# Performance work log

Measured on AMD Instinct MI355X. Metric: run time of the kernel, lower is better.

Reference implementation:

```python
import jax, jax.numpy as jnp
import numpy as np

NEG_SLOPE = 0.2


def _gatv2_layer(x, Wl, bl, Wr, br, att, bo, src, dst, N):
    """PyG GATv2Conv: lin_l on source, lin_r on target, segment softmax over dst."""
    H, C = att.shape
    xl = (x @ Wl + bl).reshape(N, H, C)  # source transform
    xr = (x @ Wr + br).reshape(N, H, C)  # target transform
    e = jax.nn.leaky_relu(xl[src] + xr[dst], NEG_SLOPE)      # [E,H,C]
    score = jnp.einsum('ehc,hc->eh', e, att)                 # [E,H]
    smax = jax.lax.stop_gradient(
        jax.ops.segment_max(score, dst, num_segments=N))     # [N,H]
    ex = jnp.exp(score - smax[dst])
    denom = jax.ops.segment_sum(ex, dst, num_segments=N)     # [N,H]
    alpha = ex / denom[dst]                                  # [E,H]
    out = jax.ops.segment_sum(xl[src] * alpha[..., None], dst, num_segments=N)
    return out.reshape(N, H * C) + bo, alpha


def setup_inputs() -> dict:
    key = jax.random.key(0)
    ks = jax.random.split(key, 24)
    N, E, F_in, Hd, H = 50000, 800000, 16, 128, 4
    C = Hd // H

    def p(k, shape, scale=0.05):
        return jax.random.normal(k, shape, jnp.float32) * scale

    inp = {
        'x': jax.random.normal(ks[0], (N, F_in), jnp.float32),
        'edge_index': jax.random.randint(ks[1], (2, E), 0, N, jnp.int32),
        'edge_attr': jax.random.normal(ks[2], (E, 4), jnp.float32),
        'batch': jnp.zeros((N,), jnp.int32),
        'enc_W': p(ks[3], (F_in, Hd)), 'enc_b': p(ks[4], (Hd,)),
        'g1_Wl': p(ks[5], (Hd, Hd)), 'g1_bl': p(ks[6], (Hd,)),
        'g1_Wr': p(ks[7], (Hd, Hd)), 'g1_br': p(ks[8], (Hd,)),
        'g1_att': p(ks[9], (H, C)), 'g1_bo': p(ks[10], (Hd,)),
        'g2_Wl': p(ks[11], (Hd, Hd)), 'g2_bl': p(ks[12], (Hd,)),
        'g2_Wr': p(ks[13], (Hd, Hd)), 'g2_br': p(ks[14], (Hd,)),
        'g2_att': p(ks[15], (H, C)), 'g2_bo': p(ks[16], (Hd,)),
        'mlp_W1': p(ks[17], (Hd, Hd)), 'mlp_b1': p(ks[18], (Hd,)),
        'mlp_W2': p(ks[19], (Hd, 1)), 'mlp_b2': p(ks[20], (1,)),
    }
    return inp


def reference(x, edge_index, edge_attr, batch,
              enc_W, enc_b,
              g1_Wl, g1_bl, g1_Wr, g1_br, g1_att, g1_bo,
              g2_Wl, g2_bl, g2_Wr, g2_br, g2_att, g2_bo,
              mlp_W1, mlp_b1, mlp_W2, mlp_b2):
    N = x.shape[0]
    # add_self_loops=True (both GAT layers)
    loops = jnp.arange(N, dtype=edge_index.dtype)
    src = jnp.concatenate([edge_index[0], loops])
    dst = jnp.concatenate([edge_index[1], loops])

    h = x @ enc_W + enc_b                                    # node_encoder
    h1, a1 = _gatv2_layer(h, g1_Wl, g1_bl, g1_Wr, g1_br, g1_att, g1_bo, src, dst, N)
    h1 = jax.nn.relu(h1)
    h2, a2 = _gatv2_layer(h1, g2_Wl, g2_bl, g2_Wr, g2_br, g2_att, g2_bo, src, dst, N)
    logits = jax.nn.relu(h2 @ mlp_W1 + mlp_b1) @ mlp_W2 + mlp_b2  # [N,1]
    probs = jax.nn.sigmoid(logits[:, 0])                     # [N]
    return probs, (a1, a2)
```

## Files before the change

### kernel.cpp

```cpp
#include <hip/hip_runtime.h>
#include <hip/hip_bf16.h>

#define NEG_SLOPE 0.2f
#define AS 136
#define CAPD 64
#define L2E 1.44269504f
#define EPB 4096

typedef __bf16 bf16x8 __attribute__((ext_vector_type(8)));
typedef float  f32x4  __attribute__((ext_vector_type(4)));

__device__ __forceinline__ float b2f(__hip_bfloat16 v) { return __bfloat162float(v); }
__device__ __forceinline__ __hip_bfloat16 f2b(float v) { return __float2bfloat16(v); }
__device__ __forceinline__ float lo16(unsigned u) { return __uint_as_float(u << 16); }
__device__ __forceinline__ float hi16(unsigned u) { return __uint_as_float(u & 0xFFFF0000u); }

template<int CTRL>
__device__ __forceinline__ float dpp_add(float p) {
    int t = __builtin_amdgcn_update_dpp(0, __float_as_int(p), CTRL, 0xF, 0xF, true);
    return p + __int_as_float(t);
}

__device__ __forceinline__ float fexp2(float x) {
    float r;
    asm("v_exp_f32 %0, %1" : "=v"(r) : "v"(x));
    return r;
}

__device__ __forceinline__ int wild16(unsigned short w) {
    int e = (w >> 7) & 0xFF;
    return (e == 0 || e >= 0xC0) ? 1 : 0;
}

__device__ __forceinline__ void store_out(void* out, size_t idx, float v, int isF32) {
    if (isF32) ((float*)out)[idx] = v;
    else       ((__hip_bfloat16*)out)[idx] = f2b(v);
}

#define NCVT 13
struct CvtTab {
    const void* src[NCVT];
    float*      dst[NCVT];
    int         n[NCVT];
    int         total;
};
struct WtTab { const void* src[5]; __hip_bfloat16* dst[5]; };

__global__ __launch_bounds__(1024) void k_pre(const int* __restrict__ ei, int E,
        int ET, int N, int shift, int nbkt, int b1, int* __restrict__ gcnt,
        CvtTab tab, WtTab wt, const unsigned short* __restrict__ det,
        int* __restrict__ FLAG) {
    __shared__ int shp[1024];
    __shared__ __hip_bfloat16 wst[1024];
    int t = threadIdx.x, b = blockIdx.x;
    if (b < b1) {
        if (t < 512) shp[t] = 0;
        __syncthreads();
        int e0 = b * EPB, e1 = min(e0 + EPB, ET);
        for (int e = e0 + t; e < e1; e += 1024) {
            int d = (e < E) ? ei[E + e] : (e - E);
            if ((unsigned)d < (unsigned)N) atomicAdd(&shp[d >> shift], 1);
        }
        __syncthreads();
        for (int i = t; i < nbkt; i += 1024) gcnt[(size_t)i * b1 + b] = shp[i];
        return;
    }
    shp[t] = wild16(det[t * 2]);
    __syncthreads();
    for (int off = 512; off >= 1; off >>= 1) {
        if (t < off) shp[t] += shp[t + off];
        __syncthreads();
    }
    int isF32 = shp[0] > 128;
    int j = b - b1;
    if (j < 80) {
        if (j == 0 && t == 0) *FLAG = isF32;
        int kl = t >> 7;
        int m  = j >> 4;
        int k0 = (j & 15) * 8;
        int k  = k0 + kl, c = t & 127;
        float v = isF32 ? ((const float*)wt.src[m])[k * 128 + c]
                        : b2f(((const __hip_bfloat16*)wt.src[m])[k * 128 + c]);
        wst[c * 8 + kl] = f2b(v);
        __syncthreads();
        if (t < 128)
            *((uint4*)(wt.dst[m] + t * 128 + k0)) = ((const uint4*)wst)[t];
    } else {
        int i = (j - 80) * 1024 + t;
        if (i >= tab.total) return;
        int seg = 0, rem = i;
        while (rem >= tab.n[seg]) { rem -= tab.n[seg]; ++seg; }
        float v = isF32 ? ((const float*)tab.src[seg])[rem]
                        : b2f(((const __hip_bfloat16*)tab.src[seg])[rem]);
        tab.dst[seg][rem] = v;
    }
}

__global__ __launch_bounds__(256) void k_scanA(const int* __restrict__ cnt, int M,
                                               int* __restrict__ out, int* __restrict__ bsum) {
    __shared__ int sh[256];
    int t = threadIdx.x, i = blockIdx.x * 256 + t;
    int v = (i < M) ? cnt[i] : 0;
    sh[t] = v;
    __syncthreads();
    for (int off = 1; off < 256; off <<= 1) {
        int u = (t >= off) ? sh[t - off] : 0;
        __syncthreads();
        sh[t] += u;
        __syncthreads();
    }
    if (i < M) out[i] = sh[t] - v;
    if (t == 255) bsum[blockIdx.x] = sh[255];
}

__global__ __launch_bounds__(256) void k_binB(const int* __restrict__ ei, int E,
        int ET, int N, int shift, int nbkt, int b1, const int* __restrict__ offs,
        const int* __restrict__ bsum, int MB, int2* __restrict__ stg) {
    __shared__ int sh[256];
    __shared__ int sbex[1024];
    __shared__ int base[512];
    int t = threadIdx.x, blk = blockIdx.x;
    int carry = 0;
    for (int bs = 0; bs < MB; bs += 256) {
        int idx = bs + t;
        int vv = (idx < MB) ? bsum[idx] : 0;
        sh[t] = vv;
        __syncthreads();
        for (int off = 1; off < 256; off <<= 1) {
            int u = (t >= off) ? sh[t - off] : 0;
            __syncthreads();
            sh[t] += u;
            __syncthreads();
        }
        if (idx < MB) sbex[idx] = carry + sh[t] - vv;
        carry += sh[255];
        __syncthreads();
    }
    for (int i = t; i < nbkt; i += 256) {
        int gi = i * b1 + blk;
        base[i] = offs[gi] + sbex[gi >> 8];
    }
    __syncthreads();
    int mask = (1 << shift) - 1;
    int e0 = blk * EPB, e1 = min(e0 + EPB, ET);
    for (int e = e0 + t; e < e1; e += 256) {
        int s, d;
        if (e < E) { s = ei[e]; d = ei[E + e]; } else { s = d = e - E; }
        if ((unsigned)d >= (unsigned)N) continue;
        int pos = atomicAdd(&base[d >> shift], 1);
        stg[pos] = make_int2(e, s | ((d & mask) << 20));
    }
}

__global__ __launch_bounds__(256) void k_csr_gemm(
        const int2* __restrict__ stg, const int* __restrict__ offs,
        const int* __restrict__ bsum, int MB, int N, int shift, int b1,
        int nbkt, int* __restrict__ rs, int2* __restrict__ pk,
        const void* __restrict__ x, const float* __restrict__ encW,
        const float* __restrict__ encb, const int* __restrict__ flag,
        const __hip_bfloat16* __restrict__ WLt, const float* __restrict__ bl,
        const __hip_bfloat16* __restrict__ WRt, const float* __restrict__ br,
        __hip_bfloat16* __restrict__ xl, __hip_bfloat16* __restrict__ xr) {
    __shared__ __align__(16) char smem[(64 + 128) * AS * 2];
    int t = threadIdx.x;
    if (blockIdx.x < nbkt) {
        int* off2 = (int*)smem;
        int* cnt2 = off2 + 512;
        int* part = cnt2 + 512;
        int* red  = part + 256;
        int bkt = blockIdx.x;
        int node0 = bkt << shift;
        int npb = 1 << shift;
        int mask = npb - 1;
        int nn = min(npb, N - node0);
        int i0 = bkt * b1, i1 = (bkt + 1) * b1;
        int c0 = i0 >> 8, c1 = i1 >> 8;
        int a0 = 0, a1 = 0, aT = 0;
        for (int bb = t; bb < MB; bb += 256) {
            int vb = bsum[bb];
            aT += vb;
            if (bb < c0) a0 += vb;
            if (bb < c1) a1 += vb;
        }
        red[t] = a0; __syncthreads();
        for (int off = 128; off >= 1; off >>= 1) { if (t < off) red[t] += red[t + off]; __syncthreads(); }
        int S0 = red[0]; __syncthreads();
        red[t] = a1; __syncthreads();
        for (int off = 128; off >= 1; off >>= 1) { if (t < off) red[t] += red[t + off]; __syncthreads(); }
        int S1 = red[0]; __syncthreads();
        red[t] = aT; __syncthreads();
        for (int off = 128; off >= 1; off >>= 1) { if (t < off) red[t] += red[t + off]; __syncthreads(); }
        int ST = red[0]; __syncthreads();
        int b0 = S0 + offs[i0];
        int bend = (bkt + 1 < nbkt) ? (S1 + offs[i1]) : ST;
        if (bkt == nbkt - 1 && t == 0) rs[N] = ST;
        int ec = bend - b0;
        for (int i = t; i < nn; i += 256) cnt2[i] = 0;
        __syncthreads();
        for (int i = t; i < ec; i += 256) {
            int2 es = stg[b0 + i];
            atomicAdd(&cnt2[(es.y >> 20) & mask], 1);
        }
        __syncthreads();
        int loc[2], sum = 0, base2 = t * 2;
#pragma unroll
        for (int k = 0; k < 2; ++k) {
            int idx = base2 + k;
            int v = (idx < nn) ? cnt2[idx] : 0;
            loc[k] = sum; sum += v;
        }
        part[t] = sum;
        __syncthreads();
        for (int off = 1; off < 256; off <<= 1) {
            int u = (t >= off) ? part[t - off] : 0;
            __syncthreads();
            part[t] += u;
            __syncthreads();
        }
        int pbase = part[t] - sum;
#pragma unroll
        for (int k = 0; k < 2; ++k) {
            int idx = base2 + k;
            if (idx < nn) {
                int p = b0 + pbase + loc[k];
                off2[idx] = p;
                rs[node0 + idx] = p;
            }
        }
        __syncthreads();
        for (int i = t; i < ec; i += 256) {
            int2 es = stg[b0 + i];
            int dof = (es.y >> 20) & mask;
            int pos = atomicAdd(&off2[dof], 1);
            pk[pos] = make_int2(es.x, es.y & 0xFFFFF);
        }
        return;
    }
    __hip_bfloat16* hA = (__hip_bfloat16*)smem;
    __hip_bfloat16* wB = hA + 64 * AS;
    float* encWs = (float*)wB;
    float* xs    = encWs + 2048;
    int rbase = (blockIdx.x - nbkt) * 64;
    int isF32 = *flag;
    for (int i = t; i < 2048; i += 256) encWs[i] = encW[i];
    for (int i = t; i < 1024; i += 256) {
        int r = i >> 4, k = i & 15, gr = rbase + r;
        float v = 0.f;
        if (gr < N)
            v = isF32 ? ((const float*)x)[(size_t)gr * 16 + k]
                      : b2f(((const __hip_bfloat16*)x)[(size_t)gr * 16 + k]);
        xs[r * 17 + k] = v;
    }
    __syncthreads();
    {
        int r = t >> 2, q = t & 3;
        float xv[16];
#pragma unroll
        for (int k = 0; k < 16; ++k) xv[k] = xs[r * 17 + k];
#pragma unroll
        for (int cc = 0; cc < 32; ++cc) {
            int c = q + cc * 4;
            float acc = encb[c];
#pragma unroll
            for (int k = 0; k < 16; ++k) acc += xv[k] * encWs[k * 128 + c];
            hA[r * AS + c] = f2b(acc);
        }
    }
    int wave = t >> 6, lane = t & 63, l16 = lane & 15, kq = lane >> 4;
#pragma unroll
    for (int pass = 0; pass < 2; ++pass) {
        const __hip_bfloat16* Wt = pass ? WRt : WLt;
        const float* bias        = pass ? br  : bl;
        __hip_bfloat16* out      = pass ? xr  : xl;
        __syncthreads();
        for (int i = t; i < 2048; i += 256) {
            int c = i >> 4, seg = i & 15;
            ((uint4*)(wB + c * AS))[seg] = ((const uint4*)(Wt + c * 128))[seg];
        }
        __syncthreads();
        f32x4 acc[8];
#pragma unroll
        for (int i = 0; i < 8; ++i) acc[i] = (f32x4){0.f, 0.f, 0.f, 0.f};
#pragma unroll
        for (int ks = 0; ks < 4; ++ks) {
            int kofs = ks * 32 + kq * 8;
            bf16x8 a = *(const bf16x8*)(hA + (wave * 16 + l16) * AS + kofs);
#pragma unroll
            for (int cb = 0; cb < 8; ++cb) {
                bf16x8 b = *(const bf16x8*)(wB + (cb * 16 + l16) * AS + kofs);
                acc[cb] = __builtin_amdgcn_mfma_f32_16x16x32_bf16(a, b, acc[cb], 0, 0, 0);
            }
        }
#pragma unroll
        for (int cb = 0; cb < 8; ++cb) {
            int c = cb * 16 + l16;
            float bc = bias[c];
#pragma unroll
            for (int i = 0; i < 4; ++i) {
                int r = rbase + wave * 16 + kq * 4 + i;
                if (r < N) out[(size_t)r * 128 + c] = f2b(acc[cb][i] + bc);
            }
        }
    }
}

__global__ __launch_bounds__(256) void k_gemm2_mfma(
        const __hip_bfloat16* __restrict__ in,
        const __hip_bfloat16* __restrict__ WLt, const float* __restrict__ bl,
        const __hip_bfloat16* __restrict__ WRt, const float* __restrict__ br,
        int N, __hip_bfloat16* __restrict__ xl, __hip_bfloat16* __restrict__ xr) {
    __shared__ __hip_bfloat16 hA[64 * AS];
    __shared__ __hip_bfloat16 wB[128 * AS];
    int t = threadIdx.x, rbase = blockIdx.x * 64;
    for (int i = t; i < 1024; i += 256) {
        int r = i >> 4, seg = i & 15;
        int gr = rbase + r;
        uint4 v = {0u, 0u, 0u, 0u};
        if (gr < N) v = ((const uint4*)(in + (size_t)gr * 128))[seg];
        ((uint4*)(hA + r * AS))[seg] = v;
    }
    int wave = t >> 6, lane = t & 63, l16 = lane & 15, kq = lane >> 4;
#pragma unroll
    for (int pass = 0; pass < 2; ++pass) {
        const __hip_bfloat16* Wt = pass ? WRt : WLt;
        const float* bias        = pass ? br  : bl;
        __hip_bfloat16* out      = pass ? xr  : xl;
        __syncthreads();
        for (int i = t; i < 2048; i += 256) {
            int c = i >> 4, seg = i & 15;
            ((uint4*)(wB + c * AS))[seg] = ((const uint4*)(Wt + c * 128))[seg];
        }
        __syncthreads();
        f32x4 acc[8];
#pragma unroll
        for (int i = 0; i < 8; ++i) acc[i] = (f32x4){0.f, 0.f, 0.f, 0.f};
#pragma unroll
        for (int ks = 0; ks < 4; ++ks) {
            int kofs = ks * 32 + kq * 8;
            bf16x8 a = *(const bf16x8*)(hA + (wave * 16 + l16) * AS + kofs);
#pragma unroll
            for (int cb = 0; cb < 8; ++cb) {
                bf16x8 b = *(const bf16x8*)(wB + (cb * 16 + l16) * AS + kofs);
                acc[cb] = __builtin_amdgcn_mfma_f32_16x16x32_bf16(a, b, acc[cb], 0, 0, 0);
            }
        }
#pragma unroll
        for (int cb = 0; cb < 8; ++cb) {
            int c = cb * 16 + l16;
            float bc = bias[c];
#pragma unroll
            for (int i = 0; i < 4; ++i) {
                int r = rbase + wave * 16 + kq * 4 + i;
                if (r < N) out[(size_t)r * 128 + c] = f2b(acc[cb][i] + bc);
            }
        }
    }
}

__global__ __launch_bounds__(256) void k_mlp_mfma(
        const __hip_bfloat16* __restrict__ h2, const __hip_bfloat16* __restrict__ W1t,
        const float* __restrict__ b1, const float* __restrict__ W2,
        const float* __restrict__ b2, int N,
        void* __restrict__ d_out, const int* __restrict__ flag) {
    __shared__ __hip_bfloat16 hA[64 * AS];
    __shared__ __hip_bfloat16 wB[128 * AS];
    int t = threadIdx.x, rbase = blockIdx.x * 64;
    for (int i = t; i < 2048; i += 256) {
        int c = i >> 4, seg = i & 15;
        ((uint4*)(wB + c * AS))[seg] = ((const uint4*)(W1t + c * 128))[seg];
    }
    for (int i = t; i < 1024; i += 256) {
        int r = i >> 4, seg = i & 15;
        int gr = rbase + r;
        uint4 v = {0u, 0u, 0u, 0u};
        if (gr < N) v = ((const uint4*)(h2 + (size_t)gr * 128))[seg];
        ((uint4*)(hA + r * AS))[seg] = v;
    }
    __syncthreads();
    int wave = t >> 6, lane = t & 63, l16 = lane & 15, kq = lane >> 4;
    f32x4 acc[8];
#pragma unroll
    for (int i = 0; i < 8; ++i) acc[i] = (f32x4){0.f, 0.f, 0.f, 0.f};
#pragma unroll
    for (int ks = 0; ks < 4; ++ks) {
        int kofs = ks * 32 + kq * 8;
        bf16x8 a = *(const bf16x8*)(hA + (wave * 16 + l16) * AS + kofs);
#pragma unroll
        for (int cb = 0; cb < 8; ++cb) {
            bf16x8 b = *(const bf16x8*)(wB + (cb * 16 + l16) * AS + kofs);
            acc[cb] = __builtin_amdgcn_mfma_f32_16x16x32_bf16(a, b, acc[cb], 0, 0, 0);
        }
    }
    float p[4] = {0.f, 0.f, 0.f, 0.f};
#pragma unroll
    for (int cb = 0; cb < 8; ++cb) {
        int c = cb * 16 + l16;
        float bb = b1[c], w = W2[c];
#pragma unroll
        for (int i = 0; i < 4; ++i) p[i] += fmaxf(acc[cb][i] + bb, 0.f) * w;
    }
#pragma unroll
    for (int i = 0; i < 4; ++i) {
        p[i] += __shfl_xor(p[i], 8, 16);
        p[i] += __shfl_xor(p[i], 4, 16);
        p[i] += __shfl_xor(p[i], 2, 16);
        p[i] += __shfl_xor(p[i], 1, 16);
    }
    if (l16 == 0) {
        int isF32 = *flag;
        float bb = b2[0];
#pragma unroll
        for (int i = 0; i < 4; ++i) {
            int r = rbase + wave * 16 + kq * 4 + i;
            if (r < N)
                store_out(d_out, (size_t)r,
                          1.f / (1.f + __expf(-(p[i] + bb))), isF32);
        }
    }
}

__global__ __launch_bounds__(64) void k_gat_fused(
        const __hip_bfloat16* __restrict__ xl,
        const __hip_bfloat16* __restrict__ xr,
        const int* __restrict__ rs, const int2* __restrict__ pk, int N,
        const float* __restrict__ att, const float* __restrict__ bo, int relu,
        float* __restrict__ EX2,
        void* __restrict__ alpha_out, size_t aoff, const int* __restrict__ flag,
        __hip_bfloat16* __restrict__ hout) {
    __shared__ float exsh[CAPD * 4];
    int lane = threadIdx.x;
    int n = blockIdx.x;
    if (n >= N) return;
    int h = lane >> 4, l16 = lane & 15, c0 = lane * 2;
    unsigned uxr = ((const unsigned*)(xr + (size_t)n * 128))[lane];
    float xr0 = lo16(uxr), xr1 = hi16(uxr);
    float a0 = att[c0] * L2E, a1 = att[c0 + 1] * L2E;
    float a06 = 0.6f * a0, a04 = 0.4f * a0;
    float a16 = 0.6f * a1, a14 = 0.4f * a1;
    int beg = __builtin_amdgcn_readfirstlane(rs[n]);
    int end = __builtin_amdgcn_readfirstlane(rs[n + 1]);
    const char* xlb = (const char*)xl;
    const int* pks = (const int*)pk;
    int lb = lane << 2;
    float den = 0.f, acc0 = 0.f, acc1 = 0.f;
    int r = beg;
    __builtin_amdgcn_s_setprio(1);

#define GAT_BATCH(W) { \
    unsigned u[W]; float p[W]; \
    _Pragma("unroll") \
    for (int j = 0; j < W; ++j) { \
        unsigned s = min((unsigned)(pks[((r + j) << 1) | 1] & 0xFFFFF), (unsigned)(N - 1)); \
        u[j] = *(const unsigned*)(xlb + ((size_t)s << 8) + lb); \
    } \
    _Pragma("unroll") \
    for (int j = 0; j < W; ++j) { \
        float v0 = lo16(u[j]) + xr0, v1 = hi16(u[j]) + xr1; \
        float tt = fmaf(fabsf(v0), a04, v0 * a06); \
        tt = fmaf(v1, a16, tt); \
        p[j] = fmaf(fabsf(v1), a14, tt); \
    } \
    _Pragma("unroll") \
    for (int j = 0; j < W; ++j) { \
        p[j] = dpp_add<0x121>(p[j]); \
        p[j] = dpp_add<0x122>(p[j]); \
        p[j] = dpp_add<0x124>(p[j]); \
        p[j] = dpp_add<0x128>(p[j]); \
        p[j] = fexp2(__builtin_amdgcn_fmed3f(p[j], -43.f, 43.f)); \
    } \
    if (l16 == 0) { \
        _Pragma("unroll") \
        for (int j = 0; j < W; ++j) { \
            int idx = r + j - beg; \
            if (idx < CAPD) exsh[idx * 4 + h] = p[j]; \
            else            EX2[(size_t)(r + j) * 4 + h] = p[j]; \
        } \
    } \
    _Pragma("unroll") \
    for (int j = 0; j < W; ++j) { \
        den  += p[j]; \
        acc0 = fmaf(p[j], lo16(u[j]), acc0); \
        acc1 = fmaf(p[j], hi16(u[j]), acc1); \
    } \
    r += W; }

    while (r + 8 <= end) GAT_BATCH(8)
    if (r + 4 <= end) GAT_BATCH(4)
    if (r + 2 <= end) GAT_BATCH(2)
    if (r < end) GAT_BATCH(1)
#undef GAT_BATCH
    __builtin_amdgcn_s_setprio(0);

    float invn = 1.f / fmaxf(den, 1e-30f);
    float v0 = acc0 * invn + bo[c0], v1 = acc1 * invn + bo[c0 + 1];
    if (relu) { v0 = fmaxf(v0, 0.f); v1 = fmaxf(v1, 0.f); }
    __hip_bfloat16 h0 = f2b(v0), h1 = f2b(v1);
    ushort2 st;
    st.x = *(unsigned short*)&h0;
    st.y = *(unsigned short*)&h1;
    ((ushort2*)(hout + (size_t)n * 128))[lane] = st;
    int isF32 = *flag;
    for (int r0 = beg; r0 < end; r0 += 16) {
        int rr = r0 + l16;
        if (rr < end) {
            int idx = rr - beg;
            float ex = (idx < CAPD) ? exsh[idx * 4 + h]
                                    : EX2[(size_t)rr * 4 + h];
            int e = pk[rr].x;
            store_out(alpha_out, aoff + (size_t)e * 4 + h, ex * invn, isF32);
        }
    }
}

extern "C" void kernel_launch(void* const* d_in, const int* in_sizes, int n_in,
                              void* d_out, int out_size, void* d_ws, size_t ws_size,
                              hipStream_t stream) {
    const int* ei = (const int*)d_in[1];
    const int N  = in_sizes[0] / 16;
    const int E  = in_sizes[1] / 2;
    const int ET = E + N;

    int shift = 7;
    while (((N + (1 << shift) - 1) >> shift) > 512) ++shift;
    const int nbkt = (N + (1 << shift) - 1) >> shift;
    const int B1   = (ET + EPB - 1) / EPB;
    const int M    = nbkt * B1;
    const int MB   = (M + 255) / 256;

    float* P = (float*)d_ws;
    float* encW = P; P += 2048;  float* encb = P; P += 128;
    float* b1l  = P; P += 128;   float* b1r  = P; P += 128;
    float* att1 = P; P += 128;   float* bo1  = P; P += 128;
    float* b2l  = P; P += 128;   float* b2r  = P; P += 128;
    float* att2 = P; P += 128;   float* bo2  = P; P += 128;
    float* mb1  = P; P += 128;   float* mW2  = P; P += 128;
    float* mb2  = P; P += 4;
    int*  FLAG  = (int*)P; P += 4;
    int*  RS    = (int*)P; P += N + 1;
    int*  GCNT  = (int*)P; P += M;
    int*  OFFS  = (int*)P; P += M;
    int*  BSUM  = (int*)P; P += MB;
    P = (float*)(((uintptr_t)P + 7) & ~(uintptr_t)7);
    int2* PK    = (int2*)P; P += (size_t)ET * 2;
    float* EX2  = P; P += (size_t)ET * 4;
    int2* STG   = (int2*)EX2;
    P = (float*)(((uintptr_t)P + 255) & ~(uintptr_t)255);
    __hip_bfloat16* W1Lt = (__hip_bfloat16*)P;
    __hip_bfloat16* W1Rt = W1Lt + 16384;
    __hip_bfloat16* W2Lt = W1Rt + 16384;
    __hip_bfloat16* W2Rt = W2Lt + 16384;
    __hip_bfloat16* MW1t = W2Rt + 16384;
    __hip_bfloat16* Hb   = MW1t + 16384;
    __hip_bfloat16* XL   = Hb + (size_t)N * 128;
    __hip_bfloat16* XR   = XL + (size_t)N * 128;

    CvtTab tab;
    const int srcIdx[NCVT] = {4, 5, 7, 9, 10, 11, 13, 15, 16, 17, 19, 20, 21};
    float* dsts[NCVT] = {encW, encb, b1l, b1r, att1, bo1, b2l, b2r, att2, bo2, mb1, mW2, mb2};
    const int ns[NCVT] = {2048, 128, 128, 128, 128, 128, 128, 128, 128, 128, 128, 128, 1};
    int tot = 0;
    for (int i = 0; i < NCVT; ++i) {
        tab.src[i] = d_in[srcIdx[i]];
        tab.dst[i] = dsts[i];
        tab.n[i] = ns[i];
        tot += ns[i];
    }
    tab.total = tot;
    WtTab wt;
    wt.src[0] = d_in[6];  wt.dst[0] = W1Lt;
    wt.src[1] = d_in[8];  wt.dst[1] = W1Rt;
    wt.src[2] = d_in[12]; wt.dst[2] = W2Lt;
    wt.src[3] = d_in[14]; wt.dst[3] = W2Rt;
    wt.src[4] = d_in[18]; wt.dst[4] = MW1t;
    const unsigned short* det = (const unsigned short*)d_in[4];
    const int preGrid = B1 + 80 + (tot + 1023) / 1024;
    k_pre<<<preGrid, 1024, 0, stream>>>(ei, E, ET, N, shift, nbkt, B1, GCNT,
                                        tab, wt, det, FLAG);

    const int gGrid = (N + 63) / 64;
    k_scanA<<<MB, 256, 0, stream>>>(GCNT, M, OFFS, BSUM);
    k_binB<<<B1, 256, 0, stream>>>(ei, E, ET, N, shift, nbkt, B1, OFFS, BSUM, MB, STG);
    k_csr_gemm<<<nbkt + gGrid, 256, 0, stream>>>(
        STG, OFFS, BSUM, MB, N, shift, B1, nbkt, RS, PK,
        d_in[0], encW, encb, FLAG, W1Lt, b1l, W1Rt, b1r, XL, XR);

    const size_t a1_off = (size_t)N;
    const size_t a2_off = (size_t)N + (size_t)ET * 4;

    k_gat_fused<<<N, 64, 0, stream>>>(XL, XR, RS, PK, N, att1, bo1, 1,
                                      EX2, d_out, a1_off, FLAG, Hb);

    k_gemm2_mfma<<<gGrid, 256, 0, stream>>>(Hb, W2Lt, b2l, W2Rt, b2r, N, XL, XR);
    k_gat_fused<<<N, 64, 0, stream>>>(XL, XR, RS, PK, N, att2, bo2, 0,
                                      EX2, d_out, a2_off, FLAG, Hb);

    k_mlp_mfma<<<gGrid, 256, 0, stream>>>(Hb, MW1t, mb1, mW2, mb2, N, d_out, FLAG);
}
```

Measured before the change: 301.4 us.

## Fuse GAT layers, second GEMM and MLP into one persistent kernel with grid barriers

Replaces four tail launches (GAT layer 1, layer-2 GEMM, GAT layer 2, MLP) with a single persistent kernel of 1024 blocks that loops over nodes and tiles and separates phases with atomic grid barriers. Each wave handles one node per GAT iteration, and the GEMM tiles stage weights in two 64-column halves to halve shared memory so more blocks stay resident. The aim is to remove launch gaps and tail effects between the phases. The cost is barrier spin overhead and lower per-phase parallelism, and the barriers deadlock if not all 1024 blocks can be co-resident.

Measured after the change: 879.5 us. 192% more time.

```diff
diff --git a/kernel.cpp b/kernel.cpp
--- a/kernel.cpp
+++ b/kernel.cpp
@@ -6,6 +6,7 @@
 #define CAPD 64
 #define L2E 1.44269504f
 #define EPB 4096
+#define TB  1024
 
 typedef __bf16 bf16x8 __attribute__((ext_vector_type(8)));
 typedef float  f32x4  __attribute__((ext_vector_type(4)));
@@ -35,6 +36,16 @@
 __device__ __forceinline__ void store_out(void* out, size_t idx, float v, int isF32) {
     if (isF32) ((float*)out)[idx] = v;
     else       ((__hip_bfloat16*)out)[idx] = f2b(v);
+}
+
+__device__ __forceinline__ void gridbar(int* bar, int nblk) {
+    __syncthreads();
+    if (threadIdx.x == 0) {
+        __hip_atomic_fetch_add(bar, 1, __ATOMIC_RELEASE, __HIP_MEMORY_SCOPE_AGENT);
+        while (__hip_atomic_load(bar, __ATOMIC_ACQUIRE, __HIP_MEMORY_SCOPE_AGENT) < nblk)
+            __builtin_amdgcn_s_sleep(1);
+    }
+    __syncthreads();
 }
 
 #define NCVT 13
@@ -49,7 +60,7 @@
 __global__ __launch_bounds__(1024) void k_pre(const int* __restrict__ ei, int E,
         int ET, int N, int shift, int nbkt, int b1, int* __restrict__ gcnt,
         CvtTab tab, WtTab wt, const unsigned short* __restrict__ det,
-        int* __restrict__ FLAG) {
+        int* __restrict__ FLAG, int* __restrict__ BAR) {
     __shared__ int shp[1024];
     __shared__ __hip_bfloat16 wst[1024];
     int t = threadIdx.x, b = blockIdx.x;
@@ -75,6 +86,7 @@
     int j = b - b1;
     if (j < 80) {
         if (j == 0 && t == 0) *FLAG = isF32;
+        if (j == 0 && t < 8) BAR[t] = 0;
         int kl = t >> 7;
         int m  = j >> 4;
         int k0 = (j & 15) * 8;
@@ -304,133 +316,13 @@
     }
 }
 
-__global__ __launch_bounds__(256) void k_gemm2_mfma(
-        const __hip_bfloat16* __restrict__ in,
-        const __hip_bfloat16* __restrict__ WLt, const float* __restrict__ bl,
-        const __hip_bfloat16* __restrict__ WRt, const float* __restrict__ br,
-        int N, __hip_bfloat16* __restrict__ xl, __hip_bfloat16* __restrict__ xr) {
-    __shared__ __hip_bfloat16 hA[64 * AS];
-    __shared__ __hip_bfloat16 wB[128 * AS];
-    int t = threadIdx.x, rbase = blockIdx.x * 64;
-    for (int i = t; i < 1024; i += 256) {
-        int r = i >> 4, seg = i & 15;
-        int gr = rbase + r;
-        uint4 v = {0u, 0u, 0u, 0u};
-        if (gr < N) v = ((const uint4*)(in + (size_t)gr * 128))[seg];
-        ((uint4*)(hA + r * AS))[seg] = v;
-    }
-    int wave = t >> 6, lane = t & 63, l16 = lane & 15, kq = lane >> 4;
-#pragma unroll
-    for (int pass = 0; pass < 2; ++pass) {
-        const __hip_bfloat16* Wt = pass ? WRt : WLt;
-        const float* bias        = pass ? br  : bl;
-        __hip_bfloat16* out      = pass ? xr  : xl;
-        __syncthreads();
-        for (int i = t; i < 2048; i += 256) {
-            int c = i >> 4, seg = i & 15;
-            ((uint4*)(wB + c * AS))[seg] = ((const uint4*)(Wt + c * 128))[seg];
-        }
-        __syncthreads();
-        f32x4 acc[8];
-#pragma unroll
-        for (int i = 0; i < 8; ++i) acc[i] = (f32x4){0.f, 0.f, 0.f, 0.f};
-#pragma unroll
-        for (int ks = 0; ks < 4; ++ks) {
-            int kofs = ks * 32 + kq * 8;
-            bf16x8 a = *(const bf16x8*)(hA + (wave * 16 + l16) * AS + kofs);
-#pragma unroll
-            for (int cb = 0; cb < 8; ++cb) {
-                bf16x8 b = *(const bf16x8*)(wB + (cb * 16 + l16) * AS + kofs);
-                acc[cb] = __builtin_amdgcn_mfma_f32_16x16x32_bf16(a, b, acc[cb], 0, 0, 0);
-            }
-        }
-#pragma unroll
-        for (int cb = 0; cb < 8; ++cb) {
-            int c = cb * 16 + l16;
-            float bc = bias[c];
-#pragma unroll
-            for (int i = 0; i < 4; ++i) {
-                int r = rbase + wave * 16 + kq * 4 + i;
-                if (r < N) out[(size_t)r * 128 + c] = f2b(acc[cb][i] + bc);
-            }
-        }
-    }
-}
-
-__global__ __launch_bounds__(256) void k_mlp_mfma(
-        const __hip_bfloat16* __restrict__ h2, const __hip_bfloat16* __restrict__ W1t,
-        const float* __restrict__ b1, const float* __restrict__ W2,
-        const float* __restrict__ b2, int N,
-        void* __restrict__ d_out, const int* __restrict__ flag) {
-    __shared__ __hip_bfloat16 hA[64 * AS];
-    __shared__ __hip_bfloat16 wB[128 * AS];
-    int t = threadIdx.x, rbase = blockIdx.x * 64;
-    for (int i = t; i < 2048; i += 256) {
-        int c = i >> 4, seg = i & 15;
-        ((uint4*)(wB + c * AS))[seg] = ((const uint4*)(W1t + c * 128))[seg];
-    }
-    for (int i = t; i < 1024; i += 256) {
-        int r = i >> 4, seg = i & 15;
-        int gr = rbase + r;
-        uint4 v = {0u, 0u, 0u, 0u};
-        if (gr < N) v = ((const uint4*)(h2 + (size_t)gr * 128))[seg];
-        ((uint4*)(hA + r * AS))[seg] = v;
-    }
-    __syncthreads();
-    int wave = t >> 6, lane = t & 63, l16 = lane & 15, kq = lane >> 4;
-    f32x4 acc[8];
-#pragma unroll
-    for (int i = 0; i < 8; ++i) acc[i] = (f32x4){0.f, 0.f, 0.f, 0.f};
-#pragma unroll
-    for (int ks = 0; ks < 4; ++ks) {
-        int kofs = ks * 32 + kq * 8;
-        bf16x8 a = *(const bf16x8*)(hA + (wave * 16 + l16) * AS + kofs);
-#pragma unroll
-        for (int cb = 0; cb < 8; ++cb) {
-            bf16x8 b = *(const bf16x8*)(wB + (cb * 16 + l16) * AS + kofs);
-            acc[cb] = __builtin_amdgcn_mfma_f32_16x16x32_bf16(a, b, acc[cb], 0, 0, 0);
-        }
-    }
-    float p[4] = {0.f, 0.f, 0.f, 0.f};
-#pragma unroll
-    for (int cb = 0; cb < 8; ++cb) {
-        int c = cb * 16 + l16;
-        float bb = b1[c], w = W2[c];
-#pragma unroll
-        for (int i = 0; i < 4; ++i) p[i] += fmaxf(acc[cb][i] + bb, 0.f) * w;
-    }
-#pragma unroll
-    for (int i = 0; i < 4; ++i) {
-        p[i] += __shfl_xor(p[i], 8, 16);
-        p[i] += __shfl_xor(p[i], 4, 16);
-        p[i] += __shfl_xor(p[i], 2, 16);
-        p[i] += __shfl_xor(p[i], 1, 16);
-    }
-    if (l16 == 0) {
-        int isF32 = *flag;
-        float bb = b2[0];
-#pragma unroll
-        for (int i = 0; i < 4; ++i) {
-            int r = rbase + wave * 16 + kq * 4 + i;
-            if (r < N)
-                store_out(d_out, (size_t)r,
-                          1.f / (1.f + __expf(-(p[i] + bb))), isF32);
-        }
-    }
-}
-
-__global__ __launch_bounds__(64) void k_gat_fused(
-        const __hip_bfloat16* __restrict__ xl,
-        const __hip_bfloat16* __restrict__ xr,
+
+__device__ __forceinline__ void gat_one(
+        const __hip_bfloat16* __restrict__ xl, const __hip_bfloat16* __restrict__ xr,
         const int* __restrict__ rs, const int2* __restrict__ pk, int N,
         const float* __restrict__ att, const float* __restrict__ bo, int relu,
-        float* __restrict__ EX2,
-        void* __restrict__ alpha_out, size_t aoff, const int* __restrict__ flag,
-        __hip_bfloat16* __restrict__ hout) {
-    __shared__ float exsh[CAPD * 4];
-    int lane = threadIdx.x;
-    int n = blockIdx.x;
-    if (n >= N) return;
+        float* __restrict__ EX2, void* __restrict__ alpha_out, size_t aoff,
+        int isF32, __hip_bfloat16* __restrict__ hout, float* exsh, int n, int lane) {
     int h = lane >> 4, l16 = lane & 15, c0 = lane * 2;
     unsigned uxr = ((const unsigned*)(xr + (size_t)n * 128))[lane];
     float xr0 = lo16(uxr), xr1 = hi16(uxr);
@@ -499,7 +391,6 @@
     st.x = *(unsigned short*)&h0;
     st.y = *(unsigned short*)&h1;
     ((ushort2*)(hout + (size_t)n * 128))[lane] = st;
-    int isF32 = *flag;
     for (int r0 = beg; r0 < end; r0 += 16) {
         int rr = r0 + l16;
         if (rr < end) {
@@ -510,6 +401,170 @@
             store_out(alpha_out, aoff + (size_t)e * 4 + h, ex * invn, isF32);
         }
     }
+}
+
+__device__ __forceinline__ void gemm_tile_h(
+        const __hip_bfloat16* __restrict__ in,
+        const __hip_bfloat16* __restrict__ WLt, const float* __restrict__ bl,
+        const __hip_bfloat16* __restrict__ WRt, const float* __restrict__ br,
+        int N, __hip_bfloat16* __restrict__ xl, __hip_bfloat16* __restrict__ xr,
+        int tile, __hip_bfloat16* hA, __hip_bfloat16* wB) {
+    int t = threadIdx.x, rbase = tile * 64;
+    __syncthreads();
+    for (int i = t; i < 1024; i += 256) {
+        int r = i >> 4, seg = i & 15;
+        int gr = rbase + r;
+        uint4 v = {0u, 0u, 0u, 0u};
+        if (gr < N) v = ((const uint4*)(in + (size_t)gr * 128))[seg];
+        ((uint4*)(hA + r * AS))[seg] = v;
+    }
+    int wave = t >> 6, lane = t & 63, l16 = lane & 15, kq = lane >> 4;
+#pragma unroll
+    for (int pass = 0; pass < 2; ++pass) {
+        const __hip_bfloat16* Wt = pass ? WRt : WLt;
+        const float* bias        = pass ? br  : bl;
+        __hip_bfloat16* out      = pass ? xr  : xl;
+        f32x4 acc[8];
+#pragma unroll
+        for (int i = 0; i < 8; ++i) acc[i] = (f32x4){0.f, 0.f, 0.f, 0.f};
+#pragma unroll
+        for (int half = 0; half < 2; ++half) {
+            __syncthreads();
+            for (int i = t; i < 1024; i += 256) {
+                int c = i >> 4, seg = i & 15;
+                ((uint4*)(wB + c * AS))[seg] =
+                    ((const uint4*)(Wt + (half * 64 + c) * 128))[seg];
+            }
+            __syncthreads();
+#pragma unroll
+            for (int ks = 0; ks < 4; ++ks) {
+                int kofs = ks * 32 + kq * 8;
+                bf16x8 a = *(const bf16x8*)(hA + (wave * 16 + l16) * AS + kofs);
+#pragma unroll
+                for (int cb = 0; cb < 4; ++cb) {
+                    bf16x8 b = *(const bf16x8*)(wB + (cb * 16 + l16) * AS + kofs);
+                    acc[half * 4 + cb] =
+                        __builtin_amdgcn_mfma_f32_16x16x32_bf16(a, b, acc[half * 4 + cb], 0, 0, 0);
+                }
+            }
+        }
+#pragma unroll
+        for (int q = 0; q < 8; ++q) {
+            int c = q * 16 + l16;
+            float bc = bias[c];
+#pragma unroll
+            for (int i = 0; i < 4; ++i) {
+                int r = rbase + wave * 16 + kq * 4 + i;
+                if (r < N) out[(size_t)r * 128 + c] = f2b(acc[q][i] + bc);
+            }
+        }
+    }
+}
+
+__device__ __forceinline__ void mlp_tile_h(
+        const __hip_bfloat16* __restrict__ h2, const __hip_bfloat16* __restrict__ W1t,
+        const float* __restrict__ b1, const float* __restrict__ W2,
+        const float* __restrict__ b2, int N, void* __restrict__ d_out,
+        int isF32, int tile, __hip_bfloat16* hA, __hip_bfloat16* wB) {
+    int t = threadIdx.x, rbase = tile * 64;
+    __syncthreads();
+    for (int i = t; i < 1024; i += 256) {
+        int r = i >> 4, seg = i & 15;
+        int gr = rbase + r;
+        uint4 v = {0u, 0u, 0u, 0u};
+        if (gr < N) v = ((const uint4*)(h2 + (size_t)gr * 128))[seg];
+        ((uint4*)(hA + r * AS))[seg] = v;
+    }
+    int wave = t >> 6, lane = t & 63, l16 = lane & 15, kq = lane >> 4;
+    f32x4 acc[8];
+#pragma unroll
+    for (int i = 0; i < 8; ++i) acc[i] = (f32x4){0.f, 0.f, 0.f, 0.f};
+#pragma unroll
+    for (int half = 0; half < 2; ++half) {
+        __syncthreads();
+        for (int i = t; i < 1024; i += 256) {
+            int c = i >> 4, seg = i & 15;
+            ((uint4*)(wB + c * AS))[seg] =
+                ((const uint4*)(W1t + (half * 64 + c) * 128))[seg];
+        }
+        __syncthreads();
+#pragma unroll
+        for (int ks = 0; ks < 4; ++ks) {
+            int kofs = ks * 32 + kq * 8;
+            bf16x8 a = *(const bf16x8*)(hA + (wave * 16 + l16) * AS + kofs);
+#pragma unroll
+            for (int cb = 0; cb < 4; ++cb) {
+                bf16x8 b = *(const bf16x8*)(wB + (cb * 16 + l16) * AS + kofs);
+                acc[half * 4 + cb] =
+                    __builtin_amdgcn_mfma_f32_16x16x32_bf16(a, b, acc[half * 4 + cb], 0, 0, 0);
+            }
+        }
+    }
+    float p[4] = {0.f, 0.f, 0.f, 0.f};
+#pragma unroll
+    for (int q = 0; q < 8; ++q) {
+        int c = q * 16 + l16;
+        float bb = b1[c], w = W2[c];
+#pragma unroll
+        for (int i = 0; i < 4; ++i) p[i] += fmaxf(acc[q][i] + bb, 0.f) * w;
+    }
+#pragma unroll
+    for (int i = 0; i < 4; ++i) {
+        p[i] += __shfl_xor(p[i], 8, 16);
+        p[i] += __shfl_xor(p[i], 4, 16);
+        p[i] += __shfl_xor(p[i], 2, 16);
+        p[i] += __shfl_xor(p[i], 1, 16);
+    }
+    if (l16 == 0) {
+        float bb = b2[0];
+#pragma unroll
+        for (int i = 0; i < 4; ++i) {
+            int r = rbase + wave * 16 + kq * 4 + i;
+            if (r < N)
+                store_out(d_out, (size_t)r,
+                          1.f / (1.f + __expf(-(p[i] + bb))), isF32);
+        }
+    }
+}
+
+__global__ __launch_bounds__(256, 4) void k_tail(
+        const __hip_bfloat16* __restrict__ XL, const __hip_bfloat16* __restrict__ XR,
+        const int* __restrict__ rs, const int2* __restrict__ pk, int N, int gtiles,
+        const float* __restrict__ att1, const float* __restrict__ bo1,
+        const float* __restrict__ att2, const float* __restrict__ bo2,
+        float* __restrict__ EX2, void* __restrict__ d_out,
+        size_t a1_off, size_t a2_off, const int* __restrict__ flag,
+        __hip_bfloat16* __restrict__ Hb,
+        const __hip_bfloat16* __restrict__ W2Lt, const float* __restrict__ b2l,
+        const __hip_bfloat16* __restrict__ W2Rt, const float* __restrict__ b2r,
+        const __hip_bfloat16* __restrict__ MW1t, const float* __restrict__ mb1,
+        const float* __restrict__ mW2, const float* __restrict__ mb2,
+        int* __restrict__ BAR) {
+    __shared__ __align__(16) char smem[64 * AS * 2 * 2];
+    __hip_bfloat16* hA = (__hip_bfloat16*)smem;
+    __hip_bfloat16* wB = hA + 64 * AS;
+    int t = threadIdx.x, wv = t >> 6, lane = t & 63;
+    int isF32 = *flag;
+    int gw = blockIdx.x * 4 + wv;
+    float* exsh = (float*)smem + wv * CAPD * 4;
+
+    for (int n = gw; n < N; n += TB * 4)
+        gat_one(XL, XR, rs, pk, N, att1, bo1, 1, EX2, d_out, a1_off, isF32,
+                Hb, exsh, n, lane);
+    gridbar(&BAR[0], TB);
+
+    for (int tile = blockIdx.x; tile < gtiles; tile += TB)
+        gemm_tile_h(Hb, W2Lt, b2l, W2Rt, b2r, N, (__hip_bfloat16*)XL,
+                    (__hip_bfloat16*)XR, tile, hA, wB);
+    gridbar(&BAR[1], TB);
+
+    for (int n = gw; n < N; n += TB * 4)
+        gat_one(XL, XR, rs, pk, N, att2, bo2, 0, EX2, d_out, a2_off, isF32,
+                Hb, exsh, n, lane);
+    gridbar(&BAR[2], TB);
+
+    for (int tile = blockIdx.x; tile < gtiles; tile += TB)
+        mlp_tile_h(Hb, MW1t, mb1, mW2, mb2, N, d_out, isF32, tile, hA, wB);
 }
 
 extern "C" void kernel_launch(void* const* d_in, const int* in_sizes, int n_in,
@@ -536,6 +591,7 @@
     float* mb1  = P; P += 128;   float* mW2  = P; P += 128;
     float* mb2  = P; P += 4;
     int*  FLAG  = (int*)P; P += 4;
+    int*  BAR   = (int*)P; P += 8;
     int*  RS    = (int*)P; P += N + 1;
     int*  GCNT  = (int*)P; P += M;
     int*  OFFS  = (int*)P; P += M;
@@ -575,7 +631,7 @@
     const unsigned short* det = (const unsigned short*)d_in[4];
     const int preGrid = B1 + 80 + (tot + 1023) / 1024;
     k_pre<<<preGrid, 1024, 0, stream>>>(ei, E, ET, N, shift, nbkt, B1, GCNT,
-                                        tab, wt, det, FLAG);
+                                        tab, wt, det, FLAG, BAR);
 
     const int gGrid = (N + 63) / 64;
     k_scanA<<<MB, 256, 0, stream>>>(GCNT, M, OFFS, BSUM);
@@ -587,12 +643,9 @@
     const size_t a1_off = (size_t)N;
     const size_t a2_off = (size_t)N + (size_t)ET * 4;
 
-    k_gat_fused<<<N, 64, 0, stream>>>(XL, XR, RS, PK, N, att1, bo1, 1,
-                                      EX2, d_out, a1_off, FLAG, Hb);
-
-    k_gemm2_mfma<<<gGrid, 256, 0, stream>>>(Hb, W2Lt, b2l, W2Rt, b2r, N, XL, XR);
-    k_gat_fused<<<N, 64, 0, stream>>>(XL, XR, RS, PK, N, att2, bo2, 0,
-                                      EX2, d_out, a2_off, FLAG, Hb);
-
-    k_mlp_mfma<<<gGrid, 256, 0, stream>>>(Hb, MW1t, mb1, mW2, mb2, N, d_out, FLAG);
-}
+    k_tail<<<TB, 256, 0, stream>>>(XL, XR, RS, PK, N, gGrid,
+                                   att1, bo1, att2, bo2, EX2, d_out,
+                                   a1_off, a2_off, FLAG, Hb,
+                                   W2Lt, b2l, W2Rt, b2r,
+                                   MW1t, mb1, mW2, mb2, BAR);
+}
```

## Fold global scan into binning kernel and precompute bucket bounds

Applied to the files above, without the earlier changes.

Removes the separate scan kernel and has each binning block recompute per-bucket prefix sums directly from the count matrix (row sums plus the prefix up to its own block), then exclusively scans the bucket totals. Block 0 writes the bucket boundary array that the CSR kernel now reads directly, replacing that kernel's three block reductions over the block sums. This saves a launch and redundant reductions, but every binning block now reads the whole count matrix (nbkt*B1 ints) serially per bucket row.

New measurement: 354.5 us. 1.18x slower.

```diff
diff --git a/kernel.cpp b/kernel.cpp
--- a/kernel.cpp
+++ b/kernel.cpp
@@ -96,50 +96,53 @@
     }
 }
 
-__global__ __launch_bounds__(256) void k_scanA(const int* __restrict__ cnt, int M,
-                                               int* __restrict__ out, int* __restrict__ bsum) {
-    __shared__ int sh[256];
-    int t = threadIdx.x, i = blockIdx.x * 256 + t;
-    int v = (i < M) ? cnt[i] : 0;
-    sh[t] = v;
+__global__ __launch_bounds__(256) void k_binB(const int* __restrict__ ei, int E,
+        int ET, int N, int shift, int nbkt, int b1, const int* __restrict__ gcnt,
+        int2* __restrict__ stg, int* __restrict__ bb, int* __restrict__ rs) {
+    __shared__ int rowpre[512];
+    __shared__ int rsum[512];
+    __shared__ int base[512];
+    __shared__ int part[256];
+    int t = threadIdx.x, blk = blockIdx.x;
+    for (int i = t; i < nbkt; i += 256) {
+        const int* row = gcnt + (size_t)i * b1;
+        int sum = 0, pre = 0;
+        for (int bp = 0; bp < b1; ++bp) {
+            int v = row[bp];
+            if (bp == blk) pre = sum;
+            sum += v;
+        }
+        rowpre[i] = pre;
+        rsum[i] = sum;
+    }
+    __syncthreads();
+    int loc[2], sum2 = 0, base2 = t * 2;
+#pragma unroll
+    for (int k = 0; k < 2; ++k) {
+        int idx = base2 + k;
+        int v = (idx < nbkt) ? rsum[idx] : 0;
+        loc[k] = sum2; sum2 += v;
+    }
+    part[t] = sum2;
     __syncthreads();
     for (int off = 1; off < 256; off <<= 1) {
-        int u = (t >= off) ? sh[t - off] : 0;
-        __syncthreads();
-        sh[t] += u;
-        __syncthreads();
-    }
-    if (i < M) out[i] = sh[t] - v;
-    if (t == 255) bsum[blockIdx.x] = sh[255];
-}
-
-__global__ __launch_bounds__(256) void k_binB(const int* __restrict__ ei, int E,
-        int ET, int N, int shift, int nbkt, int b1, const int* __restrict__ offs,
-        const int* __restrict__ bsum, int MB, int2* __restrict__ stg) {
-    __shared__ int sh[256];
-    __shared__ int sbex[1024];
-    __shared__ int base[512];
-    int t = threadIdx.x, blk = blockIdx.x;
-    int carry = 0;
-    for (int bs = 0; bs < MB; bs += 256) {
-        int idx = bs + t;
-        int vv = (idx < MB) ? bsum[idx] : 0;
-        sh[t] = vv;
-        __syncthreads();
-        for (int off = 1; off < 256; off <<= 1) {
-            int u = (t >= off) ? sh[t - off] : 0;
-            __syncthreads();
-            sh[t] += u;
-            __syncthreads();
-        }
-        if (idx < MB) sbex[idx] = carry + sh[t] - vv;
-        carry += sh[255];
-        __syncthreads();
-    }
-    for (int i = t; i < nbkt; i += 256) {
-        int gi = i * b1 + blk;
-        base[i] = offs[gi] + sbex[gi >> 8];
-    }
+        int u = (t >= off) ? part[t - off] : 0;
+        __syncthreads();
+        part[t] += u;
+        __syncthreads();
+    }
+    int pbase = part[t] - sum2;
+    int total = part[255];
+#pragma unroll
+    for (int k = 0; k < 2; ++k) {
+        int idx = base2 + k;
+        if (idx < nbkt) {
+            int bbx = pbase + loc[k];
+            base[idx] = bbx + rowpre[idx];
+            if (blk == 0) bb[idx] = bbx;
+        }
+    }
+    if (blk == 0 && t == 0) { bb[nbkt] = total; rs[N] = total; }
     __syncthreads();
     int mask = (1 << shift) - 1;
     int e0 = blk * EPB, e1 = min(e0 + EPB, ET);
@@ -153,9 +156,8 @@
 }
 
 __global__ __launch_bounds__(256) void k_csr_gemm(
-        const int2* __restrict__ stg, const int* __restrict__ offs,
-        const int* __restrict__ bsum, int MB, int N, int shift, int b1,
-        int nbkt, int* __restrict__ rs, int2* __restrict__ pk,
+        const int2* __restrict__ stg, const int* __restrict__ bb,
+        int N, int shift, int nbkt, int* __restrict__ rs, int2* __restrict__ pk,
         const void* __restrict__ x, const float* __restrict__ encW,
         const float* __restrict__ encb, const int* __restrict__ flag,
         const __hip_bfloat16* __restrict__ WLt, const float* __restrict__ bl,
@@ -167,33 +169,12 @@
         int* off2 = (int*)smem;
         int* cnt2 = off2 + 512;
         int* part = cnt2 + 512;
-        int* red  = part + 256;
         int bkt = blockIdx.x;
         int node0 = bkt << shift;
         int npb = 1 << shift;
         int mask = npb - 1;
         int nn = min(npb, N - node0);
-        int i0 = bkt * b1, i1 = (bkt + 1) * b1;
-        int c0 = i0 >> 8, c1 = i1 >> 8;
-        int a0 = 0, a1 = 0, aT = 0;
-        for (int bb = t; bb < MB; bb += 256) {
-            int vb = bsum[bb];
-            aT += vb;
-            if (bb < c0) a0 += vb;
-            if (bb < c1) a1 += vb;
-        }
-        red[t] = a0; __syncthreads();
-        for (int off = 128; off >= 1; off >>= 1) { if (t < off) red[t] += red[t + off]; __syncthreads(); }
-        int S0 = red[0]; __syncthreads();
-        red[t] = a1; __syncthreads();
-        for (int off = 128; off >= 1; off >>= 1) { if (t < off) red[t] += red[t + off]; __syncthreads(); }
-        int S1 = red[0]; __syncthreads();
-        red[t] = aT; __syncthreads();
-        for (int off = 128; off >= 1; off >>= 1) { if (t < off) red[t] += red[t + off]; __syncthreads(); }
-        int ST = red[0]; __syncthreads();
-        int b0 = S0 + offs[i0];
-        int bend = (bkt + 1 < nbkt) ? (S1 + offs[i1]) : ST;
-        if (bkt == nbkt - 1 && t == 0) rs[N] = ST;
+        int b0 = bb[bkt], bend = bb[bkt + 1];
         int ec = bend - b0;
         for (int i = t; i < nn; i += 256) cnt2[i] = 0;
         __syncthreads();
@@ -525,7 +506,6 @@
     const int nbkt = (N + (1 << shift) - 1) >> shift;
     const int B1   = (ET + EPB - 1) / EPB;
     const int M    = nbkt * B1;
-    const int MB   = (M + 255) / 256;
 
     float* P = (float*)d_ws;
     float* encW = P; P += 2048;  float* encb = P; P += 128;
@@ -537,9 +517,8 @@
     float* mb2  = P; P += 4;
     int*  FLAG  = (int*)P; P += 4;
     int*  RS    = (int*)P; P += N + 1;
+    int*  BB    = (int*)P; P += nbkt + 1;
     int*  GCNT  = (int*)P; P += M;
-    int*  OFFS  = (int*)P; P += M;
-    int*  BSUM  = (int*)P; P += MB;
     P = (float*)(((uintptr_t)P + 7) & ~(uintptr_t)7);
     int2* PK    = (int2*)P; P += (size_t)ET * 2;
     float* EX2  = P; P += (size_t)ET * 4;
@@ -578,10 +557,9 @@
                                         tab, wt, det, FLAG);
 
     const int gGrid = (N + 63) / 64;
-    k_scanA<<<MB, 256, 0, stream>>>(GCNT, M, OFFS, BSUM);
-    k_binB<<<B1, 256, 0, stream>>>(ei, E, ET, N, shift, nbkt, B1, OFFS, BSUM, MB, STG);
+    k_binB<<<B1, 256, 0, stream>>>(ei, E, ET, N, shift, nbkt, B1, GCNT, STG, BB, RS);
     k_csr_gemm<<<nbkt + gGrid, 256, 0, stream>>>(
-        STG, OFFS, BSUM, MB, N, shift, B1, nbkt, RS, PK,
+        STG, BB, N, shift, nbkt, RS, PK,
         d_in[0], encW, encb, FLAG, W1Lt, b1l, W1Rt, b1r, XL, XR);
 
     const size_t a1_off = (size_t)N;
```
